# Optimization experiments

Hardware: AMD Instinct MI355X
Metric: run time of the kernel (lower is better)

Reference implementation:

```python
import jax, jax.numpy as jnp
import numpy as np

DIM = 768
NUM_HEADS = 12
HEAD_DIM = DIM // NUM_HEADS
SCALE = HEAD_DIM ** -0.5


def setup_inputs() -> dict:
    key = jax.random.key(0)
    k1, k2, k3, k4 = jax.random.split(key, 4)
    B, N = 2, 4096
    x = jax.random.normal(k1, (B, N, DIM), dtype=jnp.float32)
    # qkv: nn.Linear(dim, 3*dim, bias=False)
    W_qkv = jax.random.normal(k2, (DIM, 3 * DIM), dtype=jnp.float32) * (DIM ** -0.5)
    # proj: nn.Linear(dim, dim) with bias
    W_proj = jax.random.normal(k3, (DIM, DIM), dtype=jnp.float32) * (DIM ** -0.5)
    b_proj = jax.random.normal(k4, (DIM,), dtype=jnp.float32) * 0.02
    return {"x": x, "W_qkv": W_qkv, "W_proj": W_proj, "b_proj": b_proj}


def reference(x, W_qkv, W_proj, b_proj):
    B, N, C = x.shape
    qkv = x @ W_qkv  # [B, N, 3C]
    qkv = qkv.reshape(B, N, 3, NUM_HEADS, HEAD_DIM)
    q = qkv[:, :, 0].transpose(0, 2, 1, 3)  # [B, H, N, D]
    k = qkv[:, :, 1].transpose(0, 2, 1, 3)
    v = qkv[:, :, 2].transpose(0, 2, 1, 3)
    attn = jnp.einsum('bhnd,bhmd->bhnm', q, k) * SCALE  # [B, H, N, N]
    attn = jax.nn.softmax(attn, axis=-1)
    out = jnp.einsum('bhnm,bhmd->bhnd', attn, v)  # [B, H, N, D]
    out = out.transpose(0, 2, 1, 3).reshape(B, N, C)
    return out @ W_proj + b_proj
```

## Files before the change

kernel.cpp:

```cpp
#include <hip/hip_runtime.h>
#include <stdint.h>

#define NBATCH 2
#define SEQ    4096
#define CDIM   768
#define NHEADS 12
#define HDIM   64
#define MTOK   (NBATCH*SEQ)
#define TC3    (3*CDIM)
#define QSCALE (0.125f * 1.4426950408889634f)
#define SMAX 12.0f

typedef unsigned short u16;
typedef __attribute__((ext_vector_type(8))) short bh8;
typedef __attribute__((ext_vector_type(4))) float f32x4;
typedef __attribute__((ext_vector_type(16))) float f32x16;
typedef __attribute__((ext_vector_type(4))) unsigned short us4;

__device__ __forceinline__ u16 f2bf(float f) {
  union { float f; uint32_t u; } v; v.f = f;
  return (u16)((v.u + 0x7FFFu + ((v.u >> 16) & 1u)) >> 16);
}

__device__ __forceinline__ uint32_t cvt_pk_bf16(float a, float b) {
  uint32_t r;
  asm("v_cvt_pk_bf16_f32 %0, %1, %2" : "=v"(r) : "v"(a), "v"(b));
  return r;
}

#define GL_LDS16(src, dst) \
  __builtin_amdgcn_global_load_lds((const __attribute__((address_space(1))) void*)(src), \
                                   (__attribute__((address_space(3))) void*)(dst), 16, 0, 0)

__global__ void cast_x_kernel(const float* __restrict__ in, u16* __restrict__ out, int n4) {
  int i = blockIdx.x * blockDim.x + threadIdx.x;
  if (i >= n4) return;
  float4 v = ((const float4*)in)[i];
  us4 o;
  o[0] = f2bf(v.x); o[1] = f2bf(v.y); o[2] = f2bf(v.z); o[3] = f2bf(v.w);
  ((us4*)out)[i] = o;
}

__global__ void transpose_cast_kernel(const float* __restrict__ in, u16* __restrict__ out,
                                      int R, int C) {
  __shared__ float t[32][33];
  int c0 = blockIdx.x * 32, r0 = blockIdx.y * 32;
  int tx = threadIdx.x, ty = threadIdx.y;
#pragma unroll
  for (int i = 0; i < 4; ++i)
    t[ty + 8 * i][tx] = in[(r0 + ty + 8 * i) * C + c0 + tx];
  __syncthreads();
#pragma unroll
  for (int i = 0; i < 4; ++i)
    out[(c0 + ty + 8 * i) * R + r0 + tx] = f2bf(t[tx][ty + 8 * i]);
}

__global__ __launch_bounds__(256) void gemm_qkv_kernel(
    const u16* __restrict__ A, const u16* __restrict__ Bt,
    u16* __restrict__ Qs, u16* __restrict__ Kb, u16* __restrict__ Vt) {
  __shared__ __align__(16) u16 As[128 * 32];
  __shared__ __align__(16) u16 Bs[128 * 32];
  int blk = blockIdx.x;
  int bm = blk / 18, bn = blk % 18;
  int m0 = bm * 128, n0 = bn * 128;
  int tid = threadIdx.x;
  int wv = tid >> 6, ln = tid & 63;
  int wr = wv >> 1, wc = wv & 1;

  f32x4 acc[4][4];
#pragma unroll
  for (int i = 0; i < 4; ++i)
#pragma unroll
    for (int j = 0; j < 4; ++j) acc[i][j] = (f32x4){0.f, 0.f, 0.f, 0.f};

  const char* Ab = (const char*)(A + m0 * CDIM);
  const char* Bb = (const char*)(Bt + n0 * CDIM);

  for (int kt = 0; kt < CDIM / 32; ++kt) {
#pragma unroll
    for (int i = 0; i < 2; ++i) {
      int idx = i * 256 + tid;
      int r = idx >> 2, c = idx & 3;
      int cs = c ^ ((r >> 1) & 3);
      GL_LDS16(Ab + r * (CDIM * 2) + kt * 64 + cs * 16, (char*)As + idx * 16);
      GL_LDS16(Bb + r * (CDIM * 2) + kt * 64 + cs * 16, (char*)Bs + idx * 16);
    }
    __syncthreads();

    bh8 af[4];
#pragma unroll
    for (int mi = 0; mi < 4; ++mi) {
      int r = 64 * wr + 16 * mi + (ln & 15);
      int cs = (ln >> 4) ^ ((r >> 1) & 3);
      af[mi] = *(const bh8*)((const char*)As + r * 64 + cs * 16);
    }
#pragma unroll
    for (int nj = 0; nj < 4; ++nj) {
      int r = 64 * wc + 16 * nj + (ln & 15);
      int cs = (ln >> 4) ^ ((r >> 1) & 3);
      bh8 bf = *(const bh8*)((const char*)Bs + r * 64 + cs * 16);
#pragma unroll
      for (int mi = 0; mi < 4; ++mi)
        acc[mi][nj] = __builtin_amdgcn_mfma_f32_16x16x32_bf16(af[mi], bf, acc[mi][nj], 0, 0, 0);
    }
    __syncthreads();
  }

  int b = m0 >> 12;
#pragma unroll
  for (int nj = 0; nj < 4; ++nj) {
    int nb = n0 + 64 * wc + 16 * nj;
    int which = nb / CDIM;
    int rem = nb % CDIM;
    int h = rem / 64;
    int d = (rem % 64) + (ln & 15);
#pragma unroll
    for (int mi = 0; mi < 4; ++mi) {
      int t0 = (m0 & 4095) + 64 * wr + 16 * mi + ((ln >> 4) << 2);
      f32x4 v = acc[mi][nj];
      if (which == 0) {
#pragma unroll
        for (int q = 0; q < 4; ++q)
          Qs[((b * 12 + h) * 4096 + t0 + q) * 64 + d] = f2bf(v[q] * QSCALE);
      } else if (which == 1) {
#pragma unroll
        for (int q = 0; q < 4; ++q)
          Kb[((b * 12 + h) * 4096 + t0 + q) * 64 + d] = f2bf(v[q]);
      } else {
        us4 o;
#pragma unroll
        for (int q = 0; q < 4; ++q) o[q] = f2bf(v[q]);
        *(us4*)(Vt + ((b * 12 + h) * 64 + d) * 4096 + t0) = o;
      }
    }
  }
}

__device__ __forceinline__ void softmax_pack(
    const f32x16& s, float& lsum, bh8& pf_lo, bh8& pf_hi) {
  float p[16];
#pragma unroll
  for (int e = 0; e < 16; ++e) { p[e] = __builtin_amdgcn_exp2f(s[e]); lsum += p[e]; }
  unsigned int W[8];
#pragma unroll
  for (int g = 0; g < 4; ++g) {
    W[2 * g]     = cvt_pk_bf16(p[4 * g],     p[4 * g + 1]);
    W[2 * g + 1] = cvt_pk_bf16(p[4 * g + 2], p[4 * g + 3]);
  }
  unsigned int a0 = W[0], a1 = W[2], b0 = W[1], b1 = W[3];
  asm("v_permlane32_swap_b32 %0, %1" : "+v"(a0), "+v"(a1));
  asm("v_permlane32_swap_b32 %0, %1" : "+v"(b0), "+v"(b1));
  unsigned int c0 = W[4], c1 = W[6], d0 = W[5], d1 = W[7];
  asm("v_permlane32_swap_b32 %0, %1" : "+v"(c0), "+v"(c1));
  asm("v_permlane32_swap_b32 %0, %1" : "+v"(d0), "+v"(d1));
  union { unsigned int u[4]; bh8 v; } u0, u1;
  u0.u[0] = a0; u0.u[1] = b0; u0.u[2] = a1; u0.u[3] = b1;
  u1.u[0] = c0; u1.u[1] = d0; u1.u[2] = c1; u1.u[3] = d1;
  pf_lo = u0.v; pf_hi = u1.v;
}

__device__ __forceinline__ void attn_tile64(
    const char* kb, const char* vb, const bh8* qf,
    f32x16* od, float& lsum, int q31, int h, int x7) {
  f32x16 s0, s1;
#pragma unroll
  for (int e = 0; e < 16; ++e) { s0[e] = -SMAX; s1[e] = -SMAX; }
  __builtin_amdgcn_s_setprio(1);
#pragma unroll
  for (int ks = 0; ks < 4; ++ks) {
    int cs = ((2 * ks + h) ^ x7) * 16;
    bh8 k0 = *(const bh8*)(kb + q31 * 128 + cs);
    s0 = __builtin_amdgcn_mfma_f32_32x32x16_bf16(k0, qf[ks], s0, 0, 0, 0);
    bh8 k1 = *(const bh8*)(kb + (32 + q31) * 128 + cs);
    s1 = __builtin_amdgcn_mfma_f32_32x32x16_bf16(k1, qf[ks], s1, 0, 0, 0);
  }
  __builtin_amdgcn_s_setprio(0);

  bh8 pf[4];
  softmax_pack(s0, lsum, pf[0], pf[1]);
  softmax_pack(s1, lsum, pf[2], pf[3]);

  __builtin_amdgcn_s_setprio(1);
#pragma unroll
  for (int m = 0; m < 4; ++m) {
    int cs = ((2 * m + h) ^ x7) * 16;
    bh8 v0 = *(const bh8*)(vb + q31 * 128 + cs);
    od[0] = __builtin_amdgcn_mfma_f32_32x32x16_bf16(v0, pf[m], od[0], 0, 0, 0);
    bh8 v1 = *(const bh8*)(vb + (32 + q31) * 128 + cs);
    od[1] = __builtin_amdgcn_mfma_f32_32x32x16_bf16(v1, pf[m], od[1], 0, 0, 0);
  }
  __builtin_amdgcn_s_setprio(0);
}

__global__ __launch_bounds__(256, 3) void attn_kernel(
    const u16* __restrict__ Qs, const u16* __restrict__ Kb,
    const u16* __restrict__ Vt, u16* __restrict__ O) {
  __shared__ __align__(16) u16 Ks[2 * 64 * 64];
  __shared__ __align__(16) u16 Vs[2 * 64 * 64];
  int blk = blockIdx.x;
  int xcd = blk & 7, idx = blk >> 3;
  int bh = xcd + 8 * (idx >> 5);
  int qt = idx & 31;
  int tid = threadIdx.x, wv = tid >> 6, ln = tid & 63;
  int q31 = ln & 31, h = ln >> 5, x7 = ln & 7;

  const u16* qrow = Qs + (bh * 4096 + qt * 128 + wv * 32 + q31) * 64;
  bh8 qf[4];
#pragma unroll
  for (int ks = 0; ks < 4; ++ks)
    qf[ks] = *(const bh8*)(qrow + 16 * ks + 8 * h);

  f32x16 od[2];
#pragma unroll
  for (int e = 0; e < 16; ++e) { od[0][e] = 0.f; od[1][e] = 0.f; }
  float lsum = 0.f;

  const char* Kt0 = (const char*)(Kb + bh * 4096 * 64);
  const char* Vt0 = (const char*)(Vt + bh * 64 * 4096);

  int r0 = tid >> 3, c0 = tid & 7, cs0 = (c0 ^ (r0 & 7)) * 16;
  const char* ksrcA = Kt0 + r0 * 128 + cs0;
  const char* ksrcB = Kt0 + (r0 + 32) * 128 + cs0;
  const char* vsrcA = Vt0 + r0 * 8192 + cs0;
  const char* vsrcB = Vt0 + (r0 + 32) * 8192 + cs0;
  char* kd = (char*)Ks + tid * 16;
  char* vd = (char*)Vs + tid * 16;

  GL_LDS16(ksrcA, kd); GL_LDS16(ksrcB, kd + 4096);
  GL_LDS16(vsrcA, vd); GL_LDS16(vsrcB, vd + 4096);
  __syncthreads();

  const char* kb0 = (const char*)Ks; const char* kb1 = kb0 + 8192;
  const char* vb0 = (const char*)Vs; const char* vb1 = vb0 + 8192;

  for (int t = 0; t < 32; ++t) {
    GL_LDS16(ksrcA + (2 * t + 1) * 8192, kd + 8192);
    GL_LDS16(ksrcB + (2 * t + 1) * 8192, kd + 12288);
    GL_LDS16(vsrcA + (2 * t + 1) * 128, vd + 8192);
    GL_LDS16(vsrcB + (2 * t + 1) * 128, vd + 12288);
    attn_tile64(kb0, vb0, qf, od, lsum, q31, h, x7);
    __syncthreads();
    if (t < 31) {
      GL_LDS16(ksrcA + (2 * t + 2) * 8192, kd);
      GL_LDS16(ksrcB + (2 * t + 2) * 8192, kd + 4096);
      GL_LDS16(vsrcA + (2 * t + 2) * 128, vd);
      GL_LDS16(vsrcB + (2 * t + 2) * 128, vd + 4096);
    }
    attn_tile64(kb1, vb1, qf, od, lsum, q31, h, x7);
    __syncthreads();
  }

  float l = lsum + __shfl_xor(lsum, 32);
  float inv = 1.0f / l;

  int b = bh / 12, hd = bh % 12;
  int token = qt * 128 + wv * 32 + q31;
  u16* obase = O + (b * 4096 + token) * 768 + hd * 64;
#pragma unroll
  for (int dblk = 0; dblk < 2; ++dblk)
#pragma unroll
    for (int g = 0; g < 4; ++g) {
      us4 w;
#pragma unroll
      for (int j = 0; j < 4; ++j) w[j] = f2bf(od[dblk][4 * g + j] * inv);
      *(us4*)(obase + 32 * dblk + 8 * g + 4 * h) = w;
    }
}

__global__ __launch_bounds__(256) void gemm_proj_kernel(
    const u16* __restrict__ A, const u16* __restrict__ Bt,
    const float* __restrict__ bias, float* __restrict__ out) {
  __shared__ __align__(16) u16 As[128 * 32];
  __shared__ __align__(16) u16 Bs[128 * 32];
  int blk = blockIdx.x;
  int bm = blk / 6, bn = blk % 6;
  int m0 = bm * 128, n0 = bn * 128;
  int tid = threadIdx.x;
  int wv = tid >> 6, ln = tid & 63;
  int wr = wv >> 1, wc = wv & 1;

  f32x4 acc[4][4];
#pragma unroll
  for (int i = 0; i < 4; ++i)
#pragma unroll
    for (int j = 0; j < 4; ++j) acc[i][j] = (f32x4){0.f, 0.f, 0.f, 0.f};

  const char* Ab = (const char*)(A + m0 * CDIM);
  const char* Bb = (const char*)(Bt + n0 * CDIM);

  for (int kt = 0; kt < CDIM / 32; ++kt) {
#pragma unroll
    for (int i = 0; i < 2; ++i) {
      int idx = i * 256 + tid;
      int r = idx >> 2, c = idx & 3;
      int cs = c ^ ((r >> 1) & 3);
      GL_LDS16(Ab + r * (CDIM * 2) + kt * 64 + cs * 16, (char*)As + idx * 16);
      GL_LDS16(Bb + r * (CDIM * 2) + kt * 64 + cs * 16, (char*)Bs + idx * 16);
    }
    __syncthreads();

    bh8 af[4];
#pragma unroll
    for (int mi = 0; mi < 4; ++mi) {
      int r = 64 * wr + 16 * mi + (ln & 15);
      int cs = (ln >> 4) ^ ((r >> 1) & 3);
      af[mi] = *(const bh8*)((const char*)As + r * 64 + cs * 16);
    }
#pragma unroll
    for (int nj = 0; nj < 4; ++nj) {
      int r = 64 * wc + 16 * nj + (ln & 15);
      int cs = (ln >> 4) ^ ((r >> 1) & 3);
      bh8 bf = *(const bh8*)((const char*)Bs + r * 64 + cs * 16);
#pragma unroll
      for (int mi = 0; mi < 4; ++mi)
        acc[mi][nj] = __builtin_amdgcn_mfma_f32_16x16x32_bf16(af[mi], bf, acc[mi][nj], 0, 0, 0);
    }
    __syncthreads();
  }

#pragma unroll
  for (int nj = 0; nj < 4; ++nj) {
    int col = n0 + 64 * wc + 16 * nj + (ln & 15);
    float bv = bias[col];
#pragma unroll
    for (int mi = 0; mi < 4; ++mi) {
      int row = m0 + 64 * wr + 16 * mi + ((ln >> 4) << 2);
#pragma unroll
      for (int q = 0; q < 4; ++q)
        out[(row + q) * CDIM + col] = acc[mi][nj][q] + bv;
    }
  }
}

extern "C" void kernel_launch(void* const* d_in, const int* in_sizes, int n_in,
                              void* d_out, int out_size, void* d_ws, size_t ws_size,
                              hipStream_t stream) {
  const float* x     = (const float*)d_in[0];
  const float* Wqkv  = (const float*)d_in[1];
  const float* Wproj = (const float*)d_in[2];
  const float* bias  = (const float*)d_in[3];
  float* out = (float*)d_out;

  u16* xb   = (u16*)d_ws;
  u16* Wqt  = xb + MTOK * CDIM;
  u16* Wpt  = Wqt + TC3 * CDIM;
  u16* Qs   = Wpt + CDIM * CDIM;
  u16* Kb   = Qs + 24 * 4096 * 64;
  u16* Vt   = Kb + 24 * 4096 * 64;
  u16* attn = Vt + 24 * 64 * 4096;

  cast_x_kernel<<<6144, 256, 0, stream>>>(x, xb, (MTOK * CDIM) / 4);
  transpose_cast_kernel<<<dim3(TC3 / 32, CDIM / 32), dim3(32, 8), 0, stream>>>(Wqkv, Wqt, CDIM, TC3);
  transpose_cast_kernel<<<dim3(CDIM / 32, CDIM / 32), dim3(32, 8), 0, stream>>>(Wproj, Wpt, CDIM, CDIM);
  gemm_qkv_kernel<<<(MTOK / 128) * (TC3 / 128), 256, 0, stream>>>(xb, Wqt, Qs, Kb, Vt);
  attn_kernel<<<24 * (SEQ / 128), 256, 0, stream>>>(Qs, Kb, Vt, attn);
  gemm_proj_kernel<<<(MTOK / 128) * (CDIM / 128), 256, 0, stream>>>(attn, Wpt, bias, out);
}
```

Measured before the change: 200.4 us.

## Give each attention wave 64 query rows to reuse K/V fragments across two subtiles

The attention kernel now runs two waves per block instead of four, and each wave handles 64 query rows as two 32-row subtiles. Each K fragment is read from LDS once and used for both subtiles, and each V fragment likewise feeds two accumulators, which halves LDS reads per MFMA. Staging loads are split into four copies per thread to cover the same tile with fewer threads. The cost is more registers per wave (four output accumulators, two Q sets), fewer waves per CU, and less latency hiding.

```diff
diff --git a/kernel.cpp b/kernel.cpp
--- a/kernel.cpp
+++ b/kernel.cpp
@@ -159,40 +159,46 @@
   pf_lo = u0.v; pf_hi = u1.v;
 }
 
-__device__ __forceinline__ void attn_tile64(
-    const char* kb, const char* vb, const bh8* qf,
-    f32x16* od, float& lsum, int q31, int h, int x7) {
+__device__ __forceinline__ void attn_half(
+    const char* kb, const char* vb, const bh8* qf0, const bh8* qf1,
+    f32x16* od, float& ls0, float& ls1, int kblk,
+    int q31, int h, int x7) {
+  const char* krow = kb + (kblk * 32 + q31) * 128;
+  bh8 kf[4];
+#pragma unroll
+  for (int ks = 0; ks < 4; ++ks)
+    kf[ks] = *(const bh8*)(krow + ((2 * ks + h) ^ x7) * 16);
+
   f32x16 s0, s1;
 #pragma unroll
   for (int e = 0; e < 16; ++e) { s0[e] = -SMAX; s1[e] = -SMAX; }
   __builtin_amdgcn_s_setprio(1);
 #pragma unroll
   for (int ks = 0; ks < 4; ++ks) {
-    int cs = ((2 * ks + h) ^ x7) * 16;
-    bh8 k0 = *(const bh8*)(kb + q31 * 128 + cs);
-    s0 = __builtin_amdgcn_mfma_f32_32x32x16_bf16(k0, qf[ks], s0, 0, 0, 0);
-    bh8 k1 = *(const bh8*)(kb + (32 + q31) * 128 + cs);
-    s1 = __builtin_amdgcn_mfma_f32_32x32x16_bf16(k1, qf[ks], s1, 0, 0, 0);
+    s0 = __builtin_amdgcn_mfma_f32_32x32x16_bf16(kf[ks], qf0[ks], s0, 0, 0, 0);
+    s1 = __builtin_amdgcn_mfma_f32_32x32x16_bf16(kf[ks], qf1[ks], s1, 0, 0, 0);
   }
   __builtin_amdgcn_s_setprio(0);
 
-  bh8 pf[4];
-  softmax_pack(s0, lsum, pf[0], pf[1]);
-  softmax_pack(s1, lsum, pf[2], pf[3]);
+  bh8 p0[2], p1[2];
+  softmax_pack(s0, ls0, p0[0], p0[1]);
+  softmax_pack(s1, ls1, p1[0], p1[1]);
 
   __builtin_amdgcn_s_setprio(1);
 #pragma unroll
-  for (int m = 0; m < 4; ++m) {
-    int cs = ((2 * m + h) ^ x7) * 16;
+  for (int mm = 0; mm < 2; ++mm) {
+    int cs = ((2 * (2 * kblk + mm) + h) ^ x7) * 16;
     bh8 v0 = *(const bh8*)(vb + q31 * 128 + cs);
-    od[0] = __builtin_amdgcn_mfma_f32_32x32x16_bf16(v0, pf[m], od[0], 0, 0, 0);
+    od[0] = __builtin_amdgcn_mfma_f32_32x32x16_bf16(v0, p0[mm], od[0], 0, 0, 0);
+    od[1] = __builtin_amdgcn_mfma_f32_32x32x16_bf16(v0, p1[mm], od[1], 0, 0, 0);
     bh8 v1 = *(const bh8*)(vb + (32 + q31) * 128 + cs);
-    od[1] = __builtin_amdgcn_mfma_f32_32x32x16_bf16(v1, pf[m], od[1], 0, 0, 0);
+    od[2] = __builtin_amdgcn_mfma_f32_32x32x16_bf16(v1, p0[mm], od[2], 0, 0, 0);
+    od[3] = __builtin_amdgcn_mfma_f32_32x32x16_bf16(v1, p1[mm], od[3], 0, 0, 0);
   }
   __builtin_amdgcn_s_setprio(0);
 }
 
-__global__ __launch_bounds__(256, 3) void attn_kernel(
+__global__ __launch_bounds__(128, 2) void attn_kernel(
     const u16* __restrict__ Qs, const u16* __restrict__ Kb,
     const u16* __restrict__ Vt, u16* __restrict__ O) {
   __shared__ __align__(16) u16 Ks[2 * 64 * 64];
@@ -204,66 +210,82 @@
   int tid = threadIdx.x, wv = tid >> 6, ln = tid & 63;
   int q31 = ln & 31, h = ln >> 5, x7 = ln & 7;
 
-  const u16* qrow = Qs + (bh * 4096 + qt * 128 + wv * 32 + q31) * 64;
-  bh8 qf[4];
-#pragma unroll
-  for (int ks = 0; ks < 4; ++ks)
-    qf[ks] = *(const bh8*)(qrow + 16 * ks + 8 * h);
-
-  f32x16 od[2];
-#pragma unroll
-  for (int e = 0; e < 16; ++e) { od[0][e] = 0.f; od[1][e] = 0.f; }
-  float lsum = 0.f;
+  const u16* qbase = Qs + (bh * 4096 + qt * 128 + wv * 64 + q31) * 64;
+  bh8 qf0[4], qf1[4];
+#pragma unroll
+  for (int ks = 0; ks < 4; ++ks) {
+    qf0[ks] = *(const bh8*)(qbase + 16 * ks + 8 * h);
+    qf1[ks] = *(const bh8*)(qbase + 32 * 64 + 16 * ks + 8 * h);
+  }
+
+  f32x16 od[4];
+#pragma unroll
+  for (int i = 0; i < 4; ++i)
+#pragma unroll
+    for (int e = 0; e < 16; ++e) od[i][e] = 0.f;
+  float ls0 = 0.f, ls1 = 0.f;
 
   const char* Kt0 = (const char*)(Kb + bh * 4096 * 64);
   const char* Vt0 = (const char*)(Vt + bh * 64 * 4096);
 
-  int r0 = tid >> 3, c0 = tid & 7, cs0 = (c0 ^ (r0 & 7)) * 16;
-  const char* ksrcA = Kt0 + r0 * 128 + cs0;
-  const char* ksrcB = Kt0 + (r0 + 32) * 128 + cs0;
-  const char* vsrcA = Vt0 + r0 * 8192 + cs0;
-  const char* vsrcB = Vt0 + (r0 + 32) * 8192 + cs0;
+  int tr = tid >> 3, c = tid & 7, cs16 = (c ^ (tr & 7)) * 16;
+  const char* ksrc = Kt0 + tr * 128 + cs16;
+  const char* vsrc = Vt0 + tr * 8192 + cs16;
   char* kd = (char*)Ks + tid * 16;
   char* vd = (char*)Vs + tid * 16;
 
-  GL_LDS16(ksrcA, kd); GL_LDS16(ksrcB, kd + 4096);
-  GL_LDS16(vsrcA, vd); GL_LDS16(vsrcB, vd + 4096);
+#define STAGE(tile, buf) do {                                          \
+    const char* kp_ = ksrc + (tile) * 8192;                            \
+    const char* vp_ = vsrc + (tile) * 128;                             \
+    char* kq_ = kd + (buf) * 8192;                                     \
+    char* vq_ = vd + (buf) * 8192;                                     \
+    _Pragma("unroll")                                                  \
+    for (int i_ = 0; i_ < 4; ++i_) {                                   \
+      GL_LDS16(kp_ + i_ * 2048, kq_ + i_ * 2048);                      \
+      GL_LDS16(vp_ + i_ * 131072, vq_ + i_ * 2048);                    \
+    }                                                                  \
+  } while (0)
+
+  STAGE(0, 0);
   __syncthreads();
 
   const char* kb0 = (const char*)Ks; const char* kb1 = kb0 + 8192;
   const char* vb0 = (const char*)Vs; const char* vb1 = vb0 + 8192;
 
   for (int t = 0; t < 32; ++t) {
-    GL_LDS16(ksrcA + (2 * t + 1) * 8192, kd + 8192);
-    GL_LDS16(ksrcB + (2 * t + 1) * 8192, kd + 12288);
-    GL_LDS16(vsrcA + (2 * t + 1) * 128, vd + 8192);
-    GL_LDS16(vsrcB + (2 * t + 1) * 128, vd + 12288);
-    attn_tile64(kb0, vb0, qf, od, lsum, q31, h, x7);
-    __syncthreads();
-    if (t < 31) {
-      GL_LDS16(ksrcA + (2 * t + 2) * 8192, kd);
-      GL_LDS16(ksrcB + (2 * t + 2) * 8192, kd + 4096);
-      GL_LDS16(vsrcA + (2 * t + 2) * 128, vd);
-      GL_LDS16(vsrcB + (2 * t + 2) * 128, vd + 4096);
-    }
-    attn_tile64(kb1, vb1, qf, od, lsum, q31, h, x7);
-    __syncthreads();
-  }
-
-  float l = lsum + __shfl_xor(lsum, 32);
-  float inv = 1.0f / l;
+    STAGE(2 * t + 1, 1);
+    attn_half(kb0, vb0, qf0, qf1, od, ls0, ls1, 0, q31, h, x7);
+    __builtin_amdgcn_sched_barrier(0);
+    attn_half(kb0, vb0, qf0, qf1, od, ls0, ls1, 1, q31, h, x7);
+    __syncthreads();
+    if (t < 31) STAGE(2 * t + 2, 0);
+    attn_half(kb1, vb1, qf0, qf1, od, ls0, ls1, 0, q31, h, x7);
+    __builtin_amdgcn_sched_barrier(0);
+    attn_half(kb1, vb1, qf0, qf1, od, ls0, ls1, 1, q31, h, x7);
+    __syncthreads();
+  }
+#undef STAGE
+
+  float l0 = ls0 + __shfl_xor(ls0, 32);
+  float l1 = ls1 + __shfl_xor(ls1, 32);
+  float inv0 = 1.0f / l0, inv1 = 1.0f / l1;
 
   int b = bh / 12, hd = bh % 12;
-  int token = qt * 128 + wv * 32 + q31;
-  u16* obase = O + (b * 4096 + token) * 768 + hd * 64;
-#pragma unroll
-  for (int dblk = 0; dblk < 2; ++dblk)
+  int tok0 = qt * 128 + wv * 64 + q31;
+  u16* ob0 = O + (b * 4096 + tok0) * 768 + hd * 64;
+  u16* ob1 = ob0 + 32 * 768;
+#pragma unroll
+  for (int db = 0; db < 2; ++db)
 #pragma unroll
     for (int g = 0; g < 4; ++g) {
-      us4 w;
-#pragma unroll
-      for (int j = 0; j < 4; ++j) w[j] = f2bf(od[dblk][4 * g + j] * inv);
-      *(us4*)(obase + 32 * dblk + 8 * g + 4 * h) = w;
+      us4 w0, w1;
+#pragma unroll
+      for (int j = 0; j < 4; ++j) {
+        w0[j] = f2bf(od[2 * db][4 * g + j] * inv0);
+        w1[j] = f2bf(od[2 * db + 1][4 * g + j] * inv1);
+      }
+      *(us4*)(ob0 + 32 * db + 8 * g + 4 * h) = w0;
+      *(us4*)(ob1 + 32 * db + 8 * g + 4 * h) = w1;
     }
 }
 
@@ -353,6 +375,6 @@
   transpose_cast_kernel<<<dim3(TC3 / 32, CDIM / 32), dim3(32, 8), 0, stream>>>(Wqkv, Wqt, CDIM, TC3);
   transpose_cast_kernel<<<dim3(CDIM / 32, CDIM / 32), dim3(32, 8), 0, stream>>>(Wproj, Wpt, CDIM, CDIM);
   gemm_qkv_kernel<<<(MTOK / 128) * (TC3 / 128), 256, 0, stream>>>(xb, Wqt, Qs, Kb, Vt);
-  attn_kernel<<<24 * (SEQ / 128), 256, 0, stream>>>(Qs, Kb, Vt, attn);
+  attn_kernel<<<24 * (SEQ / 128), 128, 0, stream>>>(Qs, Kb, Vt, attn);
   gemm_proj_kernel<<<(MTOK / 128) * (CDIM / 128), 256, 0, stream>>>(attn, Wpt, bias, out);
 }
```

After: 214.9 us. +7.2%, slower.

## Split attention over key halves and combine fp32 partial outputs

Applied to the files above, without the earlier changes.

Each attention block now processes half of the key/value sequence, doubling the grid to 1536 blocks and raising the launch-bounds occupancy hint. Unnormalized fp32 partial outputs and row sums are written to workspace (one half reusing the output buffer), and a new combine kernel sums them, normalizes, and casts to bf16. This aims to improve CU load balance and occupancy at the cost of extra memory traffic and an additional launch.

```diff
diff --git a/kernel.cpp b/kernel.cpp
--- a/kernel.cpp
+++ b/kernel.cpp
@@ -16,6 +16,7 @@
 typedef __attribute__((ext_vector_type(4))) float f32x4;
 typedef __attribute__((ext_vector_type(16))) float f32x16;
 typedef __attribute__((ext_vector_type(4))) unsigned short us4;
+typedef __attribute__((ext_vector_type(8))) unsigned short us8;
 
 __device__ __forceinline__ u16 f2bf(float f) {
   union { float f; uint32_t u; } v; v.f = f;
@@ -192,15 +193,18 @@
   __builtin_amdgcn_s_setprio(0);
 }
 
-__global__ __launch_bounds__(256, 3) void attn_kernel(
+__global__ __launch_bounds__(256, 5) void attn_kernel(
     const u16* __restrict__ Qs, const u16* __restrict__ Kb,
-    const u16* __restrict__ Vt, u16* __restrict__ O) {
+    const u16* __restrict__ Vt,
+    float* __restrict__ Op0, float* __restrict__ Op1, float* __restrict__ Lp) {
   __shared__ __align__(16) u16 Ks[2 * 64 * 64];
   __shared__ __align__(16) u16 Vs[2 * 64 * 64];
   int blk = blockIdx.x;
-  int xcd = blk & 7, idx = blk >> 3;
-  int bh = xcd + 8 * (idx >> 5);
-  int qt = idx & 31;
+  int xcd = blk & 7, ii = blk >> 3;
+  int bh = xcd + 8 * (ii >> 6);
+  int rem = ii & 63;
+  int h2 = rem >> 5;
+  int qt = rem & 31;
   int tid = threadIdx.x, wv = tid >> 6, ln = tid & 63;
   int q31 = ln & 31, h = ln >> 5, x7 = ln & 7;
 
@@ -215,8 +219,8 @@
   for (int e = 0; e < 16; ++e) { od[0][e] = 0.f; od[1][e] = 0.f; }
   float lsum = 0.f;
 
-  const char* Kt0 = (const char*)(Kb + bh * 4096 * 64);
-  const char* Vt0 = (const char*)(Vt + bh * 64 * 4096);
+  const char* Kt0 = (const char*)(Kb + bh * 4096 * 64) + h2 * 2048 * 128;
+  const char* Vt0 = (const char*)(Vt + bh * 64 * 4096) + h2 * 4096;
 
   int r0 = tid >> 3, c0 = tid & 7, cs0 = (c0 ^ (r0 & 7)) * 16;
   const char* ksrcA = Kt0 + r0 * 128 + cs0;
@@ -233,14 +237,14 @@
   const char* kb0 = (const char*)Ks; const char* kb1 = kb0 + 8192;
   const char* vb0 = (const char*)Vs; const char* vb1 = vb0 + 8192;
 
-  for (int t = 0; t < 32; ++t) {
+  for (int t = 0; t < 16; ++t) {
     GL_LDS16(ksrcA + (2 * t + 1) * 8192, kd + 8192);
     GL_LDS16(ksrcB + (2 * t + 1) * 8192, kd + 12288);
     GL_LDS16(vsrcA + (2 * t + 1) * 128, vd + 8192);
     GL_LDS16(vsrcB + (2 * t + 1) * 128, vd + 12288);
     attn_tile64(kb0, vb0, qf, od, lsum, q31, h, x7);
     __syncthreads();
-    if (t < 31) {
+    if (t < 15) {
       GL_LDS16(ksrcA + (2 * t + 2) * 8192, kd);
       GL_LDS16(ksrcB + (2 * t + 2) * 8192, kd + 4096);
       GL_LDS16(vsrcA + (2 * t + 2) * 128, vd);
@@ -251,20 +255,44 @@
   }
 
   float l = lsum + __shfl_xor(lsum, 32);
-  float inv = 1.0f / l;
 
   int b = bh / 12, hd = bh % 12;
   int token = qt * 128 + wv * 32 + q31;
-  u16* obase = O + (b * 4096 + token) * 768 + hd * 64;
-#pragma unroll
-  for (int dblk = 0; dblk < 2; ++dblk)
+  float* Op = h2 ? Op1 : Op0;
+  float* obase = Op + (size_t)(b * 4096 + token) * 768 + hd * 64;
+#pragma unroll
+  for (int db = 0; db < 2; ++db)
 #pragma unroll
     for (int g = 0; g < 4; ++g) {
-      us4 w;
-#pragma unroll
-      for (int j = 0; j < 4; ++j) w[j] = f2bf(od[dblk][4 * g + j] * inv);
-      *(us4*)(obase + 32 * dblk + 8 * g + 4 * h) = w;
-    }
+      float4 w;
+      w.x = od[db][4 * g + 0]; w.y = od[db][4 * g + 1];
+      w.z = od[db][4 * g + 2]; w.w = od[db][4 * g + 3];
+      *(float4*)(obase + 32 * db + 8 * g + 4 * h) = w;
+    }
+  if (h == 0) Lp[h2 * (24 * 4096) + bh * 4096 + token] = l;
+}
+
+__global__ __launch_bounds__(256) void combine_kernel(
+    const float* __restrict__ Op0, const float* __restrict__ Op1,
+    const float* __restrict__ Lp, u16* __restrict__ attn) {
+  int idx = blockIdx.x * 256 + threadIdx.x;
+  int i8 = idx * 8;
+  int row = i8 / 768;
+  int c = i8 - row * 768;
+  int hd = c >> 6;
+  int b = row >> 12, n = row & 4095;
+  int li = (b * 12 + hd) * 4096 + n;
+  float inv = 1.0f / (Lp[li] + Lp[24 * 4096 + li]);
+  float4 a0 = *(const float4*)(Op0 + i8);
+  float4 a1 = *(const float4*)(Op0 + i8 + 4);
+  float4 b0 = *(const float4*)(Op1 + i8);
+  float4 b1 = *(const float4*)(Op1 + i8 + 4);
+  us8 w;
+  w[0] = f2bf((a0.x + b0.x) * inv); w[1] = f2bf((a0.y + b0.y) * inv);
+  w[2] = f2bf((a0.z + b0.z) * inv); w[3] = f2bf((a0.w + b0.w) * inv);
+  w[4] = f2bf((a1.x + b1.x) * inv); w[5] = f2bf((a1.y + b1.y) * inv);
+  w[6] = f2bf((a1.z + b1.z) * inv); w[7] = f2bf((a1.w + b1.w) * inv);
+  *(us8*)(attn + i8) = w;
 }
 
 __global__ __launch_bounds__(256) void gemm_proj_kernel(
@@ -348,11 +376,15 @@
   u16* Kb   = Qs + 24 * 4096 * 64;
   u16* Vt   = Kb + 24 * 4096 * 64;
   u16* attn = Vt + 24 * 64 * 4096;
+  float* Op1 = (float*)(attn + MTOK * CDIM);
+  float* Lp  = Op1 + MTOK * CDIM;
+  float* Op0 = out;
 
   cast_x_kernel<<<6144, 256, 0, stream>>>(x, xb, (MTOK * CDIM) / 4);
   transpose_cast_kernel<<<dim3(TC3 / 32, CDIM / 32), dim3(32, 8), 0, stream>>>(Wqkv, Wqt, CDIM, TC3);
   transpose_cast_kernel<<<dim3(CDIM / 32, CDIM / 32), dim3(32, 8), 0, stream>>>(Wproj, Wpt, CDIM, CDIM);
   gemm_qkv_kernel<<<(MTOK / 128) * (TC3 / 128), 256, 0, stream>>>(xb, Wqt, Qs, Kb, Vt);
-  attn_kernel<<<24 * (SEQ / 128), 256, 0, stream>>>(Qs, Kb, Vt, attn);
+  attn_kernel<<<1536, 256, 0, stream>>>(Qs, Kb, Vt, Op0, Op1, Lp);
+  combine_kernel<<<(MTOK * CDIM) / (256 * 8), 256, 0, stream>>>(Op0, Op1, Lp, attn);
   gemm_proj_kernel<<<(MTOK / 128) * (CDIM / 128), 256, 0, stream>>>(attn, Wpt, bias, out);
 }
```

Result: slower. 520.7 us (+159.8%).

## Stage 128-key K/V tiles per barrier in attention kernel

Applied to the files above, without the earlier changes.

The attention loop now stages 128 keys of K and V into LDS per pipeline step instead of 64, and runs two 64-key sub-tiles between barriers. This halves the number of __syncthreads and groups the async global-to-LDS loads, so more work sits between synchronisation points. LDS per block doubles (64KB), and launch bounds drop from 3 to 2 blocks per CU, which lowers occupancy and may hurt latency hiding.

```diff
diff --git a/kernel.cpp b/kernel.cpp
--- a/kernel.cpp
+++ b/kernel.cpp
@@ -159,8 +159,8 @@
   pf_lo = u0.v; pf_hi = u1.v;
 }
 
-__device__ __forceinline__ void attn_tile64(
-    const char* kb, const char* vb, const bh8* qf,
+__device__ __forceinline__ void attn_sub64(
+    const char* kb, const char* vbs, const bh8* qf,
     f32x16* od, float& lsum, int q31, int h, int x7) {
   f32x16 s0, s1;
 #pragma unroll
@@ -184,23 +184,23 @@
 #pragma unroll
   for (int m = 0; m < 4; ++m) {
     int cs = ((2 * m + h) ^ x7) * 16;
-    bh8 v0 = *(const bh8*)(vb + q31 * 128 + cs);
+    bh8 v0 = *(const bh8*)(vbs + q31 * 256 + cs);
     od[0] = __builtin_amdgcn_mfma_f32_32x32x16_bf16(v0, pf[m], od[0], 0, 0, 0);
-    bh8 v1 = *(const bh8*)(vb + (32 + q31) * 128 + cs);
+    bh8 v1 = *(const bh8*)(vbs + (32 + q31) * 256 + cs);
     od[1] = __builtin_amdgcn_mfma_f32_32x32x16_bf16(v1, pf[m], od[1], 0, 0, 0);
   }
   __builtin_amdgcn_s_setprio(0);
 }
 
-__global__ __launch_bounds__(256, 3) void attn_kernel(
+__global__ __launch_bounds__(256, 2) void attn_kernel(
     const u16* __restrict__ Qs, const u16* __restrict__ Kb,
     const u16* __restrict__ Vt, u16* __restrict__ O) {
-  __shared__ __align__(16) u16 Ks[2 * 64 * 64];
-  __shared__ __align__(16) u16 Vs[2 * 64 * 64];
+  __shared__ __align__(16) u16 Ks[2 * 128 * 64];
+  __shared__ __align__(16) u16 Vs[2 * 64 * 128];
   int blk = blockIdx.x;
-  int xcd = blk & 7, idx = blk >> 3;
-  int bh = xcd + 8 * (idx >> 5);
-  int qt = idx & 31;
+  int xcd = blk & 7, ii = blk >> 3;
+  int bh = xcd + 8 * (ii >> 5);
+  int qt = ii & 31;
   int tid = threadIdx.x, wv = tid >> 6, ln = tid & 63;
   int q31 = ln & 31, h = ln >> 5, x7 = ln & 7;
 
@@ -218,37 +218,36 @@
   const char* Kt0 = (const char*)(Kb + bh * 4096 * 64);
   const char* Vt0 = (const char*)(Vt + bh * 64 * 4096);
 
-  int r0 = tid >> 3, c0 = tid & 7, cs0 = (c0 ^ (r0 & 7)) * 16;
-  const char* ksrcA = Kt0 + r0 * 128 + cs0;
-  const char* ksrcB = Kt0 + (r0 + 32) * 128 + cs0;
-  const char* vsrcA = Vt0 + r0 * 8192 + cs0;
-  const char* vsrcB = Vt0 + (r0 + 32) * 8192 + cs0;
+  int kr = tid >> 3, kc = tid & 7;
+  const char* ksrc = Kt0 + kr * 128 + ((kc ^ (kr & 7)) * 16);
+  int vr = tid >> 4, vc = tid & 15;
+  const char* vsrc = Vt0 + vr * 8192 + (((vc & 8) | ((vc & 7) ^ (vr & 7))) * 16);
   char* kd = (char*)Ks + tid * 16;
   char* vd = (char*)Vs + tid * 16;
 
-  GL_LDS16(ksrcA, kd); GL_LDS16(ksrcB, kd + 4096);
-  GL_LDS16(vsrcA, vd); GL_LDS16(vsrcB, vd + 4096);
+#define STAGE_P(tile, buf) do {                                              \
+    _Pragma("unroll")                                                        \
+    for (int i_ = 0; i_ < 4; ++i_) {                                         \
+      GL_LDS16(ksrc + (tile) * 16384 + i_ * 4096,                            \
+               kd + (buf) * 16384 + i_ * 4096);                              \
+      GL_LDS16(vsrc + (tile) * 256 + i_ * 131072,                            \
+               vd + (buf) * 16384 + i_ * 4096);                              \
+    }                                                                        \
+  } while (0)
+
+  STAGE_P(0, 0);
   __syncthreads();
 
-  const char* kb0 = (const char*)Ks; const char* kb1 = kb0 + 8192;
-  const char* vb0 = (const char*)Vs; const char* vb1 = vb0 + 8192;
-
   for (int t = 0; t < 32; ++t) {
-    GL_LDS16(ksrcA + (2 * t + 1) * 8192, kd + 8192);
-    GL_LDS16(ksrcB + (2 * t + 1) * 8192, kd + 12288);
-    GL_LDS16(vsrcA + (2 * t + 1) * 128, vd + 8192);
-    GL_LDS16(vsrcB + (2 * t + 1) * 128, vd + 12288);
-    attn_tile64(kb0, vb0, qf, od, lsum, q31, h, x7);
-    __syncthreads();
-    if (t < 31) {
-      GL_LDS16(ksrcA + (2 * t + 2) * 8192, kd);
-      GL_LDS16(ksrcB + (2 * t + 2) * 8192, kd + 4096);
-      GL_LDS16(vsrcA + (2 * t + 2) * 128, vd);
-      GL_LDS16(vsrcB + (2 * t + 2) * 128, vd + 4096);
-    }
-    attn_tile64(kb1, vb1, qf, od, lsum, q31, h, x7);
-    __syncthreads();
-  }
+    int cur = t & 1;
+    if (t < 31) STAGE_P(t + 1, cur ^ 1);
+    const char* kb = (const char*)Ks + cur * 16384;
+    const char* vb = (const char*)Vs + cur * 16384;
+    attn_sub64(kb,        vb,       qf, od, lsum, q31, h, x7);
+    attn_sub64(kb + 8192, vb + 128, qf, od, lsum, q31, h, x7);
+    __syncthreads();
+  }
+#undef STAGE_P
 
   float l = lsum + __shfl_xor(lsum, 32);
   float inv = 1.0f / l;
@@ -257,13 +256,13 @@
   int token = qt * 128 + wv * 32 + q31;
   u16* obase = O + (b * 4096 + token) * 768 + hd * 64;
 #pragma unroll
-  for (int dblk = 0; dblk < 2; ++dblk)
+  for (int db = 0; db < 2; ++db)
 #pragma unroll
     for (int g = 0; g < 4; ++g) {
       us4 w;
 #pragma unroll
-      for (int j = 0; j < 4; ++j) w[j] = f2bf(od[dblk][4 * g + j] * inv);
-      *(us4*)(obase + 32 * dblk + 8 * g + 4 * h) = w;
+      for (int j = 0; j < 4; ++j) w[j] = f2bf(od[db][4 * g + j] * inv);
+      *(us4*)(obase + 32 * db + 8 * g + 4 * h) = w;
     }
 }
 
@@ -353,6 +352,6 @@
   transpose_cast_kernel<<<dim3(TC3 / 32, CDIM / 32), dim3(32, 8), 0, stream>>>(Wqkv, Wqt, CDIM, TC3);
   transpose_cast_kernel<<<dim3(CDIM / 32, CDIM / 32), dim3(32, 8), 0, stream>>>(Wproj, Wpt, CDIM, CDIM);
   gemm_qkv_kernel<<<(MTOK / 128) * (TC3 / 128), 256, 0, stream>>>(xb, Wqt, Qs, Kb, Vt);
-  attn_kernel<<<24 * (SEQ / 128), 256, 0, stream>>>(Qs, Kb, Vt, attn);
+  attn_kernel<<<768, 256, 0, stream>>>(Qs, Kb, Vt, attn);
   gemm_proj_kernel<<<(MTOK / 128) * (CDIM / 128), 256, 0, stream>>>(attn, Wpt, bias, out);
 }
```

Result: slower. 219.2 us (+9.4%).
